# Performance work log

Hardware: AMD Instinct MI355X
Metric: run time of the kernel (lower is better)

Reference implementation:

```python
import jax, jax.numpy as jnp
import numpy as np

DIM = 768
NUM_HEADS = 12
HEAD_DIM = DIM // NUM_HEADS
SCALE = HEAD_DIM ** -0.5
B, N = 4, 2048


def setup_inputs() -> dict:
    key = jax.random.key(0)
    k1, k2, k3 = jax.random.split(key, 3)
    x = jax.random.normal(k1, (B, N, DIM), dtype=jnp.float32)
    W_qk = jax.random.normal(k2, (2 * DIM, DIM), dtype=jnp.float32) * (DIM ** -0.5)
    b_qk = jax.random.normal(k3, (2 * DIM,), dtype=jnp.float32) * 0.02
    return {"x": x, "W_qk": W_qk, "b_qk": b_qk}


def reference(x, W_qk, b_qk):
    Bb, Nn, C = x.shape
    # qk projection: [B,N,2C] -> [B,N,2,H,D] -> q,k each [B,H,N,D]
    qk = x @ W_qk.T + b_qk
    qk = qk.reshape(Bb, Nn, 2, NUM_HEADS, HEAD_DIM).transpose(2, 0, 3, 1, 4)
    q, k = qk[0], qk[1]
    # attention scores [B,H,N,N]
    attn = jnp.einsum("bhnd,bhmd->bhnm", q, k) * SCALE
    attn = jax.nn.softmax(attn, axis=-1)
    # mean over heads, then per-query diagonal -> [B,N]
    attn_weights = jnp.diagonal(attn.mean(axis=1), axis1=-2, axis2=-1)
    return attn_weights
```

## Files before the change

kernel.cpp:

```cpp
#include <hip/hip_runtime.h>
#include <math.h>


#define B_ 4
#define N_ 2048
#define H_ 12
#define D_ 64
#define C_ 768
#define TWO_C 1536
#define QSCALE 0.18033688011112043f

typedef _Float16 half8 __attribute__((ext_vector_type(8)));
typedef _Float16 half4 __attribute__((ext_vector_type(4)));
typedef float floatx4 __attribute__((ext_vector_type(4)));

#if __has_builtin(__builtin_amdgcn_exp2f)
#define EXP2(x) __builtin_amdgcn_exp2f(x)
#else
#define EXP2(x) exp2f(x)
#endif

__device__ __forceinline__ void gload_lds16(const _Float16* g, _Float16* l) {
  __builtin_amdgcn_global_load_lds(
      (const __attribute__((address_space(1))) void*)g,
      (__attribute__((address_space(3))) void*)l, 16, 0, 0);
}

#define NX4 1572864
#define NW4 294912
__global__ __launch_bounds__(256) void conv_kernel(const float* __restrict__ x,
                                                   const float* __restrict__ W,
                                                   _Float16* __restrict__ xh,
                                                   _Float16* __restrict__ wh) {
  int i = blockIdx.x * 256 + threadIdx.x;
  const float* in;
  _Float16* out;
  int idx;
  if (i < NX4) {
    in = x; out = xh; idx = i;
  } else if (i < NX4 + NW4) {
    in = W; out = wh; idx = i - NX4;
  } else {
    return;
  }
  float4 v = ((const float4*)in)[idx];
  half4 o;
  o[0] = (_Float16)v.x; o[1] = (_Float16)v.y;
  o[2] = (_Float16)v.z; o[3] = (_Float16)v.w;
  ((half4*)out)[idx] = o;
}

__global__ __launch_bounds__(256) void proj_kernel(
    const _Float16* __restrict__ xh, const _Float16* __restrict__ wh,
    const float* __restrict__ bias, _Float16* __restrict__ qh,
    _Float16* __restrict__ kh) {
  __shared__ _Float16 As[128 * 32];
  __shared__ _Float16 Bs[128 * 32];
  const int t = threadIdx.x;
  const int l = t & 63;
  const int w = t >> 6;
  const int wr = w >> 1, wc = w & 1;

  int lin = blockIdx.y * 12 + blockIdx.x;
  int swz = (lin & 7) * 96 + (lin >> 3);
  const int bm = (swz / 12) * 128;
  const int bc = (swz % 12) * 128;

  const int srow = l >> 2;
  const int schunk = (l & 3) ^ ((l >> 3) & 3);

  floatx4 acc[4][4] = {};

  for (int k0 = 0; k0 < C_; k0 += 32) {
    __syncthreads();
#pragma unroll
    for (int i = 0; i < 2; ++i) {
      int rbase = w * 32 + i * 16;
      const _Float16* ga =
          xh + (size_t)(bm + rbase + srow) * C_ + k0 + schunk * 8;
      gload_lds16(ga, As + rbase * 32);
      const _Float16* gb =
          wh + (size_t)(bc + rbase + srow) * C_ + k0 + schunk * 8;
      gload_lds16(gb, Bs + rbase * 32);
    }
    __syncthreads();

    half8 af[4], bf[4];
#pragma unroll
    for (int fr = 0; fr < 4; ++fr) {
      int row = wr * 64 + fr * 16 + (l & 15);
      int ch = (l >> 4) ^ ((row >> 1) & 3);
      af[fr] = *(const half8*)(As + row * 32 + ch * 8);
    }
#pragma unroll
    for (int fc = 0; fc < 4; ++fc) {
      int row = wc * 64 + fc * 16 + (l & 15);
      int ch = (l >> 4) ^ ((row >> 1) & 3);
      bf[fc] = *(const half8*)(Bs + row * 32 + ch * 8);
    }
#pragma unroll
    for (int fr = 0; fr < 4; ++fr)
#pragma unroll
      for (int fc = 0; fc < 4; ++fc)
        acc[fr][fc] = __builtin_amdgcn_mfma_f32_16x16x32_f16(
            af[fr], bf[fc], acc[fr][fc], 0, 0, 0);
  }

#pragma unroll
  for (int fr = 0; fr < 4; ++fr) {
#pragma unroll
    for (int fc = 0; fc < 4; ++fc) {
#pragma unroll
      for (int j = 0; j < 4; ++j) {
        int m = bm + wr * 64 + fr * 16 + ((l >> 4) << 2) + j;
        int c = bc + wc * 64 + fc * 16 + (l & 15);
        float v = acc[fr][fc][j] + bias[c];
        int b = m >> 11, n = m & (N_ - 1);
        int cc = (c < C_) ? c : c - C_;
        if (c < C_) v *= QSCALE;
        int hh = cc >> 6, d = cc & 63;
        _Float16* dst = (c < C_) ? qh : kh;
        dst[((((size_t)b * H_ + hh) * N_ + n) << 6) + d] = (_Float16)v;
      }
    }
  }
}

__global__ __launch_bounds__(256) void attn_kernel(
    const _Float16* __restrict__ qh, const _Float16* __restrict__ kh,
    float* __restrict__ part) {
  __shared__ float red[5 * 64];
  const int t = threadIdx.x;
  const int l = t & 63;
  const int w = t >> 6;

  int lin = blockIdx.x;
  int swz = (lin & 7) * 192 + (lin >> 3);
  const int qt = swz & 31;
  const int h = (swz >> 5) % 12;
  const int b = swz / 384;

  const _Float16* qb = qh + (((size_t)(b * H_ + h) * N_ + qt * 64) << 6);
  const _Float16* kb = kh + (((size_t)(b * H_ + h) * N_) << 6);

  half8 qf[4][2];
#pragma unroll
  for (int fr = 0; fr < 4; ++fr)
#pragma unroll
    for (int kd = 0; kd < 2; ++kd)
      qf[fr][kd] = *(const half8*)(qb + (size_t)(fr * 16 + (l & 15)) * 64 +
                                   kd * 32 + (l >> 4) * 8);

  const _Float16* kl = kb + (w * 16 + (l & 15)) * 64 + (l >> 4) * 8;

  float lsum[4][4] = {};
  float ed[4] = {0.f, 0.f, 0.f, 0.f};

#define LOADK(KT, K0, K1)                                      \
  {                                                            \
    const _Float16* p_ = kl + (size_t)((KT) & 31) * 4096;      \
    K0 = *(const half8*)p_;                                    \
    K1 = *(const half8*)(p_ + 32);                             \
  }

#define COMPUTE(KT, K0, K1)                                                   \
  {                                                                           \
    floatx4 acc[4] = {};                                                      \
    _Pragma("unroll") for (int fr = 0; fr < 4; ++fr) {                        \
      acc[fr] = __builtin_amdgcn_mfma_f32_16x16x32_f16(qf[fr][0], K0,         \
                                                       acc[fr], 0, 0, 0);     \
      acc[fr] = __builtin_amdgcn_mfma_f32_16x16x32_f16(qf[fr][1], K1,         \
                                                       acc[fr], 0, 0, 0);     \
    }                                                                         \
    _Pragma("unroll") for (int fr = 0; fr < 4; ++fr)                          \
        _Pragma("unroll") for (int j = 0; j < 4; ++j) {                       \
      float e = EXP2(acc[fr][j]);                                             \
      lsum[fr][j] += e;                                                       \
      if ((KT) == qt && fr == w && (l & 15) == (((l >> 4) << 2) + j))         \
        ed[j] = e;                                                            \
    }                                                                         \
  }

  half8 a0, a1, b0, b1;
  LOADK(0, a0, a1);
  for (int kt = 0; kt < 32; kt += 2) {
    LOADK(kt + 1, b0, b1);
    COMPUTE(kt, a0, a1);
    LOADK(kt + 2, a0, a1);
    COMPUTE(kt + 1, b0, b1);
  }
#undef LOADK
#undef COMPUTE

#pragma unroll
  for (int fr = 0; fr < 4; ++fr)
#pragma unroll
    for (int j = 0; j < 4; ++j)
#pragma unroll
      for (int m = 1; m < 16; m <<= 1)
        lsum[fr][j] += __shfl_xor(lsum[fr][j], m, 16);
#pragma unroll
  for (int j = 0; j < 4; ++j)
#pragma unroll
    for (int m = 1; m < 16; m <<= 1) ed[j] += __shfl_xor(ed[j], m, 16);

  float* edl = red + 256;
  if ((l & 15) == 0) {
#pragma unroll
    for (int fr = 0; fr < 4; ++fr)
#pragma unroll
      for (int j = 0; j < 4; ++j)
        red[w * 64 + fr * 16 + ((l >> 4) << 2) + j] = lsum[fr][j];
#pragma unroll
    for (int j = 0; j < 4; ++j) edl[w * 16 + ((l >> 4) << 2) + j] = ed[j];
  }
  __syncthreads();

  if (t < 64) {
    float ls = red[t] + red[64 + t] + red[128 + t] + red[192 + t];
    part[(size_t)(b * H_ + h) * N_ + qt * 64 + t] = edl[t] / ls;
  }
}

__global__ __launch_bounds__(256) void reduce_kernel(
    const float* __restrict__ part, float* __restrict__ out) {
  int g = blockIdx.x * 256 + threadIdx.x;
  if (g >= B_ * N_) return;
  int b = g >> 11, n = g & (N_ - 1);
  float s = 0.0f;
#pragma unroll
  for (int hh = 0; hh < H_; ++hh) s += part[(size_t)(b * H_ + hh) * N_ + n];
  out[g] = s * (1.0f / (float)H_);
}

extern "C" void kernel_launch(void* const* d_in, const int* in_sizes, int n_in,
                              void* d_out, int out_size, void* d_ws,
                              size_t ws_size, hipStream_t stream) {
  const float* x = (const float*)d_in[0];
  const float* W = (const float*)d_in[1];
  const float* bias = (const float*)d_in[2];
  float* out = (float*)d_out;

  char* ws = (char*)d_ws;
  _Float16* xh = (_Float16*)ws;
  _Float16* wh = (_Float16*)(ws + 12582912);
  _Float16* qh = (_Float16*)(ws + 14942208);
  _Float16* kh = (_Float16*)(ws + 27525120);
  float* part = (float*)(ws + 40108032);

  conv_kernel<<<(NX4 + NW4 + 255) / 256, 256, 0, stream>>>(x, W, xh, wh);
  proj_kernel<<<dim3(TWO_C / 128, 8192 / 128), 256, 0, stream>>>(xh, wh, bias,
                                                                 qh, kh);
  attn_kernel<<<N_ / 64 * H_ * B_, 256, 0, stream>>>(qh, kh, part);
  reduce_kernel<<<(B_ * N_ + 255) / 256, 256, 0, stream>>>(part, out);
}
```

Measured before the change: 100.2 us.

## Stage K tiles through swizzled LDS ring buffer with async global-to-LDS loads

The attention kernel used to load K fragments straight from global memory into registers, with each wave reading its own slice. It now streams each 64x64 K tile into a 4-deep LDS ring buffer using global_load_lds, keeping three tiles in flight. Explicit vmcnt waits and a barrier run every iteration, and fragments are read from XOR-swizzled LDS. The diagonal exp capture is moved out of the hot loop under a per-tile branch. This aims to hide global latency and coalesce K loads, but it adds a block-wide barrier per tile and uses 32KB of LDS, which may cut occupancy.

```diff
diff --git a/kernel.cpp b/kernel.cpp
--- a/kernel.cpp
+++ b/kernel.cpp
@@ -129,7 +129,7 @@
 __global__ __launch_bounds__(256) void attn_kernel(
     const _Float16* __restrict__ qh, const _Float16* __restrict__ kh,
     float* __restrict__ part) {
-  __shared__ float red[5 * 64];
+  __shared__ _Float16 ks[4][64 * 64];
   const int t = threadIdx.x;
   const int l = t & 63;
   const int w = t >> 6;
@@ -151,46 +151,68 @@
       qf[fr][kd] = *(const half8*)(qb + (size_t)(fr * 16 + (l & 15)) * 64 +
                                    kd * 32 + (l >> 4) * 8);
 
-  const _Float16* kl = kb + (w * 16 + (l & 15)) * 64 + (l >> 4) * 8;
+  const int lin0 = w * 64 + l;
+  const int row0 = lin0 >> 3, slot0 = lin0 & 7;
+  const int soff0 = row0 * 64 + (slot0 ^ (row0 & 7)) * 8;
+  const int lin1 = lin0 + 256;
+  const int row1 = lin1 >> 3, slot1 = lin1 & 7;
+  const int soff1 = row1 * 64 + (slot1 ^ (row1 & 7)) * 8;
+
+#define STAGE(KT)                                                   \
+  {                                                                 \
+    const _Float16* kp_ = kb + (size_t)(KT) * 4096;                 \
+    _Float16* ld_ = ks[(KT) & 3];                                   \
+    gload_lds16(kp_ + soff0, ld_ + w * 512);                        \
+    gload_lds16(kp_ + soff1, ld_ + w * 512 + 2048);                 \
+  }
+
+  const int frow = w * 16 + (l & 15);
+  const int koff0 = frow * 64 + (((l >> 4) + 0) ^ (l & 7)) * 8;
+  const int koff1 = frow * 64 + (((l >> 4) + 4) ^ (l & 7)) * 8;
 
   float lsum[4][4] = {};
   float ed[4] = {0.f, 0.f, 0.f, 0.f};
 
-#define LOADK(KT, K0, K1)                                      \
-  {                                                            \
-    const _Float16* p_ = kl + (size_t)((KT) & 31) * 4096;      \
-    K0 = *(const half8*)p_;                                    \
-    K1 = *(const half8*)(p_ + 32);                             \
-  }
-
-#define COMPUTE(KT, K0, K1)                                                   \
+  STAGE(0);
+  STAGE(1);
+  STAGE(2);
+
+#define ITER(KT, VMASM, DO_STAGE)                                             \
   {                                                                           \
+    asm volatile(VMASM ::: "memory");                                         \
+    __builtin_amdgcn_s_barrier();                                             \
+    asm volatile("" ::: "memory");                                            \
+    const _Float16* bufp = ks[(KT) & 3];                                      \
+    half8 kf0 = *(const half8*)(bufp + koff0);                                \
+    half8 kf1 = *(const half8*)(bufp + koff1);                                \
+    if (DO_STAGE) STAGE((KT) + 3);                                            \
     floatx4 acc[4] = {};                                                      \
     _Pragma("unroll") for (int fr = 0; fr < 4; ++fr) {                        \
-      acc[fr] = __builtin_amdgcn_mfma_f32_16x16x32_f16(qf[fr][0], K0,         \
+      acc[fr] = __builtin_amdgcn_mfma_f32_16x16x32_f16(qf[fr][0], kf0,        \
                                                        acc[fr], 0, 0, 0);     \
-      acc[fr] = __builtin_amdgcn_mfma_f32_16x16x32_f16(qf[fr][1], K1,         \
+      acc[fr] = __builtin_amdgcn_mfma_f32_16x16x32_f16(qf[fr][1], kf1,        \
                                                        acc[fr], 0, 0, 0);     \
     }                                                                         \
     _Pragma("unroll") for (int fr = 0; fr < 4; ++fr)                          \
         _Pragma("unroll") for (int j = 0; j < 4; ++j) {                       \
       float e = EXP2(acc[fr][j]);                                             \
       lsum[fr][j] += e;                                                       \
-      if ((KT) == qt && fr == w && (l & 15) == (((l >> 4) << 2) + j))         \
-        ed[j] = e;                                                            \
     }                                                                         \
-  }
-
-  half8 a0, a1, b0, b1;
-  LOADK(0, a0, a1);
-  for (int kt = 0; kt < 32; kt += 2) {
-    LOADK(kt + 1, b0, b1);
-    COMPUTE(kt, a0, a1);
-    LOADK(kt + 2, a0, a1);
-    COMPUTE(kt + 1, b0, b1);
-  }
-#undef LOADK
-#undef COMPUTE
+    if ((KT) == qt) {                                                         \
+      _Pragma("unroll") for (int fr = 0; fr < 4; ++fr)                        \
+          _Pragma("unroll") for (int j = 0; j < 4; ++j) {                     \
+        if (fr == w && (l & 15) == (((l >> 4) << 2) + j))                     \
+          ed[j] = EXP2(acc[fr][j]);                                           \
+      }                                                                       \
+    }                                                                         \
+  }
+
+  for (int kt = 0; kt < 29; ++kt) ITER(kt, "s_waitcnt vmcnt(4)", true);
+  ITER(29, "s_waitcnt vmcnt(4)", false);
+  ITER(30, "s_waitcnt vmcnt(2)", false);
+  ITER(31, "s_waitcnt vmcnt(0)", false);
+#undef ITER
+#undef STAGE
 
 #pragma unroll
   for (int fr = 0; fr < 4; ++fr)
@@ -204,6 +226,8 @@
 #pragma unroll
     for (int m = 1; m < 16; m <<= 1) ed[j] += __shfl_xor(ed[j], m, 16);
 
+  __builtin_amdgcn_s_barrier();
+  float* red = (float*)ks[0];
   float* edl = red + 256;
   if ((l & 15) == 0) {
 #pragma unroll
```

Result: faster. 83.17 us (-17.0%).
